# Kernel tuning notes

Measured on AMD Instinct MI355X. Metric: run time of the kernel, lower is better.

Reference implementation:

```python
import jax, jax.numpy as jnp
import numpy as np

B = 256          # graphs per batch
NN = 400         # ROI nodes per graph (N*(N-1)/2 = 79800 = input_dim)
HID = [32, 64, 128]
KS = [200, 100, 50]   # nodes kept after each TopKPooling (ratio 0.5 each)
EPS = 1e-5


def setup_inputs() -> dict:
    key = jax.random.key(0)
    ks = jax.random.split(key, 20)
    # flattened strict upper triangle of a nonnegative FC matrix per sample
    data = jax.random.uniform(ks[0], (B, NN * (NN - 1) // 2), dtype=jnp.float32)
    inp = {"data": data}
    dims = [1] + HID
    for l in range(3):
        fan_in = dims[l]
        inp[f"W{l+1}"] = jax.random.normal(ks[1 + 5 * l], (dims[l], dims[l + 1]), jnp.float32) / np.sqrt(fan_in)
        inp[f"b{l+1}"] = jnp.zeros((dims[l + 1],), jnp.float32)
        inp[f"g{l+1}"] = jnp.ones((dims[l + 1],), jnp.float32)      # BN gamma
        inp[f"be{l+1}"] = jnp.zeros((dims[l + 1],), jnp.float32)    # BN beta
        inp[f"p{l+1}"] = jax.random.normal(ks[4 + 5 * l], (dims[l + 1],), jnp.float32) * 0.1  # TopK score vector
    return inp


def _gcn_conv(A, X, W, b):
    # GCNConv with edge weights: add self loops (weight 1), symmetric D^-1/2 A D^-1/2
    n = A.shape[1]
    Al = A + jnp.eye(n, dtype=A.dtype)[None]          # (B, n, n)
    deg = Al.sum(axis=-1)                             # (B, n)
    dis = jnp.where(deg > 0, jax.lax.rsqrt(deg), 0.0)
    An = dis[:, :, None] * Al * dis[:, None, :]
    return jnp.einsum('bij,bjf->bif', An, X @ W) + b


def _block(A, X, W, b, g, be, p, k):
    # GCNConv -> ReLU -> BatchNorm(train stats) -> (dropout=identity) -> TopKPooling
    h = jax.nn.relu(_gcn_conv(A, X, W, b))
    mu = h.mean(axis=(0, 1))
    var = h.var(axis=(0, 1))
    h = (h - mu) * jax.lax.rsqrt(var + EPS) * g + be
    # TopKPooling: score = x . p / ||p||, keep top k per graph, gate by tanh(score)
    score = h @ p / jnp.linalg.norm(p)                # (B, n)
    vals, idx = jax.lax.top_k(score, k)               # (B, k)
    Xn = jnp.take_along_axis(h, idx[:, :, None], axis=1) * jnp.tanh(vals)[:, :, None]
    bi = jnp.arange(A.shape[0])[:, None, None]
    An = A[bi, idx[:, :, None], idx[:, None, :]]      # filter_adj: edges among kept nodes
    return An, Xn


def reference(data, W1, b1, g1, be1, p1, W2, b2, g2, be2, p2, W3, b3, g3, be3, p3):
    Bn = data.shape[0]
    iu0, iu1 = np.triu_indices(NN, 1)
    A = jnp.zeros((Bn, NN, NN), data.dtype).at[:, iu0, iu1].set(data)
    A = A + jnp.swapaxes(A, 1, 2)                     # symmetric FC adjacency, zero diag
    X = jnp.ones((Bn, NN, 1), data.dtype)             # initial node feature dim = 1
    A, X = _block(A, X, W1, b1, g1, be1, p1, KS[0])
    A, X = _block(A, X, W2, b2, g2, be2, p2, KS[1])
    A, X = _block(A, X, W3, b3, g3, be3, p3, KS[2])
    return X.max(axis=1)                              # global_max_pool -> (B, 128)
```

## Files before the change

### kernel.cpp

```cpp
#include <hip/hip_runtime.h>
#include <math.h>

#define BB   256
#define NN0  400
#define NE   79800
#define NTIL 28
#define EPSF 1e-5f

__device__ __forceinline__ int tri_e(int a, int c) {
  return a*(NN0-1) - ((a*(a-1))>>1) + (c - a - 1);
}

__device__ __forceinline__ size_t PRI(int b, int ti, int tj, int r) {
  return (((size_t)b*7 + ti)*7 + tj)*64 + r;
}

__device__ __forceinline__ float wave_sum(float v) {
  #pragma unroll
  for (int o = 32; o > 0; o >>= 1) v += __shfl_xor(v, o, 64);
  return v;
}

__device__ __forceinline__ void bitonic_desc(float* sc, int* si, int P) {
  const int tid = threadIdx.x;
  for (int k = 2; k <= P; k <<= 1) {
    for (int j = k >> 1; j > 0; j >>= 1) {
      __syncthreads();
      for (int i = tid; i < P; i += 256) {
        int ixj = i ^ j;
        if (ixj > i) {
          float a = sc[i], c = sc[ixj];
          int ai = si[i], ci = si[ixj];
          bool bef = (a > c) || (a == c && ai < ci);
          bool sw = ((i & k) == 0) ? !bef : bef;
          if (sw) { sc[i] = c; sc[ixj] = a; si[i] = ci; si[ixj] = ai; }
        }
      }
    }
  }
  __syncthreads();
}

__global__ __launch_bounds__(256) void k_tri_mv(
    const float* __restrict__ data, const float* __restrict__ disv,
    float* __restrict__ pr, float* __restrict__ pc) {
  __shared__ float tile[64][65];
  __shared__ float dI[64], dJ[64];
  const int q0 = blockIdx.x % 7, b = blockIdx.x / 7;
  const int tid = threadIdx.x;
  const int wave = tid >> 6, lane = tid & 63;
  const float* __restrict__ drow = data + (size_t)b*NE;
  int ti_a[4], tj_a[4];
  #pragma unroll
  for (int u = 0; u < 4; ++u) {
    int t = q0 + u*7;
    int ti = 0, rem = t;
    while (rem >= 7 - ti) { rem -= 7 - ti; ++ti; }
    ti_a[u] = ti; tj_a[u] = ti + rem;
  }
  float vreg[16];
  float rI = 0.f, rJ = 0.f;
  auto issue = [&](int u) {
    const int i0 = ti_a[u]*64, j0 = tj_a[u]*64;
    const int ni = min(64, NN0 - i0), nj = min(64, NN0 - j0);
    #pragma unroll
    for (int k = 0; k < 16; ++k) {
      const int rr = wave*16 + k;
      const int i = i0 + rr, j = j0 + lane;
      vreg[k] = 0.f;
      if (rr < ni && lane < nj && j > i) vreg[k] = drow[tri_e(i, j)];
    }
    if (disv) {
      if (tid < 64) rI = (tid < ni) ? disv[(size_t)b*NN0 + i0 + tid] : 0.f;
      else if (tid < 128) { const int c = tid-64; rJ = (c < nj) ? disv[(size_t)b*NN0 + j0 + c] : 0.f; }
    } else {
      if (tid < 64) rI = (tid < ni) ? 1.f : 0.f;
      else if (tid < 128) rJ = (tid-64 < nj) ? 1.f : 0.f;
    }
  };
  issue(0);
  #pragma unroll 1
  for (int u = 0; u < 4; ++u) {
    const int ti = ti_a[u], tj = tj_a[u];
    if (u) __syncthreads();
    #pragma unroll
    for (int k = 0; k < 16; ++k) tile[wave*16 + k][lane] = vreg[k];
    if (tid < 64) dI[tid] = rI;
    else if (tid < 128) dJ[tid-64] = rJ;
    __syncthreads();
    if (u + 1 < 4) issue(u + 1);
    {
      const int r = tid >> 2, q = tid & 3;
      float s = 0.f;
      #pragma unroll
      for (int c = 0; c < 16; ++c) s += tile[r][q*16 + c] * dJ[q*16 + c];
      s += __shfl_xor(s, 1, 64);
      s += __shfl_xor(s, 2, 64);
      if (q == 0) pr[PRI(b, ti, tj, r)] = s;
    }
    {
      const int c = tid >> 2, q = tid & 3;
      float s = 0.f;
      #pragma unroll
      for (int r = 0; r < 16; ++r) s += tile[q*16 + r][c] * dI[q*16 + r];
      s += __shfl_xor(s, 1, 64);
      s += __shfl_xor(s, 2, 64);
      if (q == 0) pc[PRI(b, ti, tj, c)] = s;
    }
  }
}

__global__ __launch_bounds__(256) void k_dis_red(
    const float* __restrict__ pr, const float* __restrict__ pc,
    float* __restrict__ dis1) {
  const int i = blockIdx.x*256 + threadIdx.x;
  const int b = i / NN0, n = i % NN0;
  const int t = n >> 6, r = n & 63;
  float acc = 1.f;
  for (int tj = t; tj < 7; ++tj) acc += pr[PRI(b, t, tj, r)];
  for (int ti = 0; ti <= t; ++ti) acc += pc[PRI(b, ti, t, r)];
  dis1[i] = rsqrtf(acc);
}

__global__ __launch_bounds__(256) void k_sfin_stats_red(
    const float* __restrict__ dis1,
    const float* __restrict__ pr, const float* __restrict__ pc,
    const float* __restrict__ W1, const float* __restrict__ b1,
    float* __restrict__ s1, float* __restrict__ part1) {
  __shared__ float sl[256];
  __shared__ float st[64];
  __shared__ float w1s[32], b1s[32];
  const int tid = threadIdx.x;
  const int i = blockIdx.x*256 + tid;
  if (tid < 32) { w1s[tid] = W1[tid]; b1s[tid] = b1[tid]; }
  if (tid < 64) st[tid] = 0.f;
  const int b = i / NN0, n = i % NN0;
  const int t = n >> 6, r = n & 63;
  float sacc = 0.f;
  for (int tj = t; tj < 7; ++tj) sacc += pr[PRI(b, t, tj, r)];
  for (int ti = 0; ti <= t; ++ti) sacc += pc[PRI(b, ti, t, r)];
  const float d = dis1[i];
  const float s = d * (d + sacc);
  s1[i] = s;
  sl[tid] = s;
  __syncthreads();
  const int f = tid & 31, sub = tid >> 5;
  const float w = w1s[f], bb = b1s[f];
  float S = 0.f, Q = 0.f;
  #pragma unroll
  for (int k = 0; k < 32; ++k) {
    const float ss = sl[sub*32 + k];
    const float h = fmaxf(ss*w + bb, 0.f);
    S += h; Q += h*h;
  }
  atomicAdd(&st[f], S);
  atomicAdd(&st[32+f], Q);
  __syncthreads();
  if (tid < 64) part1[(size_t)blockIdx.x*64 + tid] = st[tid];
}

__global__ void k_fin1(const float* __restrict__ part1, const float* __restrict__ g1,
                       const float* __restrict__ be1, const float* __restrict__ p1,
                       float* __restrict__ bn1) {
  const int tid = threadIdx.x;
  float scale = 0.f, shift = 0.f, pv = 0.f;
  if (tid < 32) {
    float S = 0.f, Q = 0.f;
    for (int blk = 0; blk < 400; ++blk) { S += part1[(size_t)blk*64 + tid]; Q += part1[(size_t)blk*64 + 32 + tid]; }
    const float N = 102400.f;
    const float mu = S / N;
    const float var = Q / N - mu*mu;
    const float inv = rsqrtf(var + EPSF);
    scale = inv * g1[tid];
    shift = be1[tid] - mu * scale;
    pv = p1[tid];
  }
  const float pn = sqrtf(wave_sum(pv*pv));
  if (tid < 32) { bn1[tid] = scale; bn1[32+tid] = shift; bn1[64+tid] = scale*pv/pn; }
  float u = (tid < 32) ? shift*pv/pn : 0.f;
  u = wave_sum(u);
  if (tid == 0) bn1[96] = u;
}

__global__ __launch_bounds__(256) void k_top1(
    const float* __restrict__ s1, const float* __restrict__ bn1,
    const float* __restrict__ W1, const float* __restrict__ b1,
    int* __restrict__ nodes2, int* __restrict__ sperm2, float* __restrict__ X2) {
  __shared__ float sc[512]; __shared__ int si[512];
  __shared__ float sS[NN0];
  __shared__ float tvs[200];
  __shared__ int nds_l[200];
  __shared__ float w1s[32], b1s[32], cfs[32], scs[32], shs[32];
  const int tid = threadIdx.x, b = blockIdx.x;
  if (tid < 32) {
    scs[tid] = bn1[tid]; shs[tid] = bn1[32+tid]; cfs[tid] = bn1[64+tid];
    w1s[tid] = W1[tid]; b1s[tid] = b1[tid];
  }
  __syncthreads();
  const float c0 = bn1[96];
  for (int i = tid; i < 512; i += 256) {
    if (i < NN0) {
      const float s = s1[(size_t)b*NN0 + i];
      sS[i] = s;
      float sco = c0;
      #pragma unroll
      for (int f = 0; f < 32; ++f) sco += fmaxf(s*w1s[f] + b1s[f], 0.f) * cfs[f];
      sc[i] = sco; si[i] = i;
    } else { sc[i] = -INFINITY; si[i] = 0x7fffffff; }
  }
  bitonic_desc(sc, si, 512);
  for (int k = tid; k < 200; k += 256) {
    tvs[k] = tanhf(sc[k]);
    nds_l[k] = si[k];
    nodes2[b*200 + k] = si[k];
  }
  __syncthreads();
  for (int o = tid; o < 6400; o += 256) {
    const int k = o >> 5, f = o & 31;
    const float s = sS[nds_l[k]];
    const float h = fmaxf(s*w1s[f] + b1s[f], 0.f);
    X2[(size_t)b*6400 + o] = (h*scs[f] + shs[f]) * tvs[k];
  }
  __syncthreads();
  if (tid < 256) {
    sc[tid] = (tid < 200) ? -(float)nds_l[tid] : -INFINITY;
    si[tid] = (tid < 200) ? tid : 0x7fffffff;
  }
  bitonic_desc(sc, si, 256);
  if (tid < 200) sperm2[b*200 + tid] = si[tid];
}

__global__ __launch_bounds__(256) void k_gatherA2(
    const float* __restrict__ data, const int* __restrict__ nodes2,
    const int* __restrict__ sperm2, float* __restrict__ A2, float* __restrict__ dis2) {
  __shared__ int nds[200], sp[200], sn[200];
  __shared__ float rowbuf[4][200];
  const int idx = blockIdx.x;
  const int r9 = idx >> 3;
  const int b = (idx & 7)*32 + r9/50;
  const int rg = r9 % 50;
  const int tid = threadIdx.x;
  if (tid < 200) { nds[tid] = nodes2[b*200 + tid]; sp[tid] = sperm2[b*200 + tid]; }
  __syncthreads();
  if (tid < 200) sn[tid] = nds[sp[tid]];
  __syncthreads();
  const int wave = tid >> 6, lane = tid & 63;
  const int i = rg*4 + wave;
  const int ni = nds[i];
  const float* __restrict__ drow = data + (size_t)b*NE;
  float accd = 0.f;
  for (int jj = lane; jj < 200; jj += 64) {
    const int sj = sn[jj];
    float v = 0.f;
    if (sj != ni) {
      const int a = min(ni, sj), c = max(ni, sj);
      v = drow[tri_e(a, c)];
    }
    rowbuf[wave][sp[jj]] = v;
    accd += v;
  }
  __syncthreads();
  for (int j = lane; j < 200; j += 64)
    A2[((size_t)b*200 + i)*200 + j] = rowbuf[wave][j];
  accd = wave_sum(accd);
  if (lane == 0) dis2[b*200 + i] = rsqrtf(1.f + accd);
}

__global__ __launch_bounds__(256) void k_Z2(
    const float* __restrict__ X2, const float* __restrict__ W2,
    const float* __restrict__ dis2, float* __restrict__ Z2) {
  __shared__ __align__(16) float xs[200*32];
  const int tid = threadIdx.x, b = blockIdx.x;
  const int f = tid & 63;
  float wr[32];
  #pragma unroll
  for (int c = 0; c < 32; ++c) wr[c] = W2[c*64 + f];
  for (int t = tid; t < 6400; t += 256) xs[t] = X2[(size_t)b*6400 + t];
  __syncthreads();
  for (int o = tid; o < 12800; o += 256) {
    const int j = o >> 6;
    float acc = 0.f;
    #pragma unroll
    for (int c4 = 0; c4 < 8; ++c4) {
      const float4 x4 = *(const float4*)&xs[(j<<5) + (c4<<2)];
      acc += x4.x*wr[c4*4] + x4.y*wr[c4*4+1] + x4.z*wr[c4*4+2] + x4.w*wr[c4*4+3];
    }
    Z2[(size_t)b*12800 + o] = dis2[b*200 + j] * acc;
  }
}

__global__ __launch_bounds__(256) void k_conv2(
    const float* __restrict__ A2, const float* __restrict__ Z2,
    const float* __restrict__ dis2, const float* __restrict__ b2,
    float* __restrict__ h2g, float* __restrict__ part2) {
  __shared__ __align__(16) float ab[40*64];
  __shared__ __align__(16) float zb[40*64];
  __shared__ float st[128];
  const int tid = threadIdx.x;
  const int b = blockIdx.x >> 2, p = blockIdx.x & 3;
  const int tx = tid & 15, ty = tid >> 4;
  if (tid < 128) st[tid] = 0.f;
  const float4 bv = *(const float4*)&b2[tx<<2];
  float acc[4][4] = {};
  #pragma unroll 1
  for (int j0 = 0; j0 < 200; j0 += 40) {
    __syncthreads();
    for (int t = tid; t < 640; t += 256) {
      const int js = t >> 4, f4 = t & 15;
      *(float4*)&zb[(js << 6) + (f4 << 2)] =
        *(const float4*)&Z2[((size_t)b*200 + (j0 + js))*64 + (f4 << 2)];
    }
    for (int t = tid; t < 640; t += 256) {
      const int js = t >> 4, c4l = t & 15;
      const int cg = (p << 6) + (c4l << 2);
      float4 v = make_float4(0.f, 0.f, 0.f, 0.f);
      if (cg < 200)
        v = *(const float4*)&A2[((size_t)b*200 + (j0 + js))*200 + cg];
      *(float4*)&ab[(js << 6) + (c4l << 2)] = v;
    }
    __syncthreads();
    #pragma unroll 2
    for (int js = 0; js < 40; ++js) {
      const float4 a4 = *(const float4*)&ab[(js << 6) + (ty << 2)];
      const float4 z4 = *(const float4*)&zb[(js << 6) + (tx << 2)];
      acc[0][0] += a4.x*z4.x; acc[0][1] += a4.x*z4.y; acc[0][2] += a4.x*z4.z; acc[0][3] += a4.x*z4.w;
      acc[1][0] += a4.y*z4.x; acc[1][1] += a4.y*z4.y; acc[1][2] += a4.y*z4.z; acc[1][3] += a4.y*z4.w;
      acc[2][0] += a4.z*z4.x; acc[2][1] += a4.z*z4.y; acc[2][2] += a4.z*z4.z; acc[2][3] += a4.z*z4.w;
      acc[3][0] += a4.w*z4.x; acc[3][1] += a4.w*z4.y; acc[3][2] += a4.w*z4.z; acc[3][3] += a4.w*z4.w;
    }
  }
  float ss[4] = {0,0,0,0}, qq[4] = {0,0,0,0};
  #pragma unroll
  for (int qr = 0; qr < 4; ++qr) {
    const int r = (p << 6) + (ty << 2) + qr;
    if (r < 200) {
      const float d = dis2[b*200 + r];
      const float4 zi = *(const float4*)&Z2[((size_t)b*200 + r)*64 + (tx << 2)];
      const float h0 = fmaxf(d*(acc[qr][0] + zi.x) + bv.x, 0.f);
      const float h1 = fmaxf(d*(acc[qr][1] + zi.y) + bv.y, 0.f);
      const float h2v = fmaxf(d*(acc[qr][2] + zi.z) + bv.z, 0.f);
      const float h3v = fmaxf(d*(acc[qr][3] + zi.w) + bv.w, 0.f);
      *(float4*)&h2g[((size_t)b*200 + r)*64 + (tx<<2)] = make_float4(h0,h1,h2v,h3v);
      ss[0]+=h0; ss[1]+=h1; ss[2]+=h2v; ss[3]+=h3v;
      qq[0]+=h0*h0; qq[1]+=h1*h1; qq[2]+=h2v*h2v; qq[3]+=h3v*h3v;
    }
  }
  #pragma unroll
  for (int qf = 0; qf < 4; ++qf) {
    atomicAdd(&st[(tx<<2)+qf], ss[qf]);
    atomicAdd(&st[64+(tx<<2)+qf], qq[qf]);
  }
  __syncthreads();
  if (tid < 128) part2[(size_t)blockIdx.x*128 + tid] = st[tid];
}

__global__ void k_fin2(const float* __restrict__ part2, const float* __restrict__ g2,
                       const float* __restrict__ be2, const float* __restrict__ p2,
                       float* __restrict__ bn2) {
  const int f = threadIdx.x;
  float S = 0.f, Q = 0.f;
  for (int blk = 0; blk < BB*4; ++blk) { S += part2[(size_t)blk*128 + f]; Q += part2[(size_t)blk*128 + 64 + f]; }
  const float N = 51200.f;
  const float mu = S/N, var = Q/N - mu*mu, inv = rsqrtf(var + EPSF);
  const float scale = inv*g2[f], shift = be2[f] - mu*scale;
  const float pv = p2[f];
  const float pn = sqrtf(wave_sum(pv*pv));
  bn2[f] = scale; bn2[64+f] = shift; bn2[128+f] = scale*pv/pn;
  const float u = wave_sum(shift*pv/pn);
  if (f == 0) bn2[192] = u;
}

__global__ __launch_bounds__(256) void k_top2(
    const float* __restrict__ h2g, const float* __restrict__ bn2,
    const int* __restrict__ nodes2, int* __restrict__ nodes3, float* __restrict__ X3) {
  __shared__ float sc[256]; __shared__ int si[256];
  const int tid = threadIdx.x, b = blockIdx.x;
  const int wave = tid >> 6, lane = tid & 63;
  const float cf = bn2[128 + lane];
  const float c20 = bn2[192];
  for (int i = wave; i < 200; i += 4) {
    float v = h2g[((size_t)b*200 + i)*64 + lane] * cf;
    v = wave_sum(v);
    if (lane == 0) { sc[i] = v + c20; si[i] = i; }
  }
  if (tid >= 200) { sc[tid] = -INFINITY; si[tid] = 0x7fffffff; }
  bitonic_desc(sc, si, 256);
  const float scale = bn2[lane], shift = bn2[64 + lane];
  for (int o = tid; o < 6400; o += 256) {
    const int k = o >> 6;
    const int idx = si[k];
    const float tv = tanhf(sc[k]);
    X3[(size_t)b*6400 + o] = (h2g[((size_t)b*200 + idx)*64 + lane] * scale + shift) * tv;
  }
  for (int k = tid; k < 100; k += 256) nodes3[b*100 + k] = nodes2[b*200 + si[k]];
}

__global__ __launch_bounds__(256) void k_gatherA3(
    const float* __restrict__ data, const int* __restrict__ nodes3,
    float* __restrict__ A3, float* __restrict__ dis3) {
  __shared__ int nds[100];
  const int b = blockIdx.x / 25, rg = blockIdx.x % 25;
  const int tid = threadIdx.x;
  if (tid < 100) nds[tid] = nodes3[b*100 + tid];
  __syncthreads();
  const int wave = tid >> 6, lane = tid & 63;
  const int i = rg*4 + wave;
  const int ni = nds[i];
  const float* __restrict__ drow = data + (size_t)b*NE;
  float accd = 0.f;
  for (int j = lane; j < 100; j += 64) {
    float v = 0.f;
    if (j != i) {
      const int nj = nds[j];
      const int a = min(ni, nj), c = max(ni, nj);
      v = drow[tri_e(a, c)];
    }
    A3[((size_t)b*100 + i)*100 + j] = v;
    accd += v;
  }
  accd = wave_sum(accd);
  if (lane == 0) dis3[b*100 + i] = rsqrtf(1.f + accd);
}

__global__ __launch_bounds__(256) void k_Z3(
    const float* __restrict__ X3, const float* __restrict__ W3,
    const float* __restrict__ dis3, float* __restrict__ Z3) {
  __shared__ __align__(16) float xs[100*64];
  const int tid = threadIdx.x, b = blockIdx.x;
  const int f = tid & 127;
  float wr[64];
  #pragma unroll
  for (int c = 0; c < 64; ++c) wr[c] = W3[c*128 + f];
  for (int t = tid; t < 6400; t += 256) xs[t] = X3[(size_t)b*6400 + t];
  __syncthreads();
  for (int o = tid; o < 12800; o += 256) {
    const int j = o >> 7;
    float acc = 0.f;
    #pragma unroll
    for (int c4 = 0; c4 < 16; ++c4) {
      const float4 x4 = *(const float4*)&xs[(j<<6) + (c4<<2)];
      acc += x4.x*wr[c4*4] + x4.y*wr[c4*4+1] + x4.z*wr[c4*4+2] + x4.w*wr[c4*4+3];
    }
    Z3[(size_t)b*12800 + o] = dis3[b*100 + j] * acc;
  }
}

__global__ __launch_bounds__(256) void k_conv3(
    const float* __restrict__ A3, const float* __restrict__ Z3,
    const float* __restrict__ dis3, const float* __restrict__ b3,
    float* __restrict__ h3g, float* __restrict__ part3) {
  __shared__ __align__(16) float z[100*128];
  __shared__ __align__(16) float ab[32*32];
  __shared__ float st[256];
  const int tid = threadIdx.x;
  const int b = blockIdx.x >> 2, p = blockIdx.x & 3;
  const int tx = tid & 31, ty = tid >> 5;
  for (int t = tid; t < 12800; t += 256) z[t] = Z3[(size_t)b*12800 + t];
  st[tid] = 0.f;
  const float4 bv = *(const float4*)&b3[tx<<2];
  float acc[4][4] = {};
  #pragma unroll 1
  for (int j0 = 0; j0 < 100; j0 += 32) {
    const int nj = (j0 + 32 <= 100) ? 32 : (100 - j0);
    __syncthreads();
    for (int t = tid; t < nj*32; t += 256) {
      const int js = t >> 5, lr = t & 31;
      const int c = (p << 5) + lr;
      ab[t] = (c < 100) ? A3[((size_t)b*100 + (j0 + js))*100 + c] : 0.f;
    }
    __syncthreads();
    for (int js = 0; js < nj; ++js) {
      const float4 a4 = *(const float4*)&ab[(js<<5) + (ty<<2)];
      const float4 z4 = *(const float4*)&z[((j0+js)<<7) + (tx<<2)];
      acc[0][0] += a4.x*z4.x; acc[0][1] += a4.x*z4.y; acc[0][2] += a4.x*z4.z; acc[0][3] += a4.x*z4.w;
      acc[1][0] += a4.y*z4.x; acc[1][1] += a4.y*z4.y; acc[1][2] += a4.y*z4.z; acc[1][3] += a4.y*z4.w;
      acc[2][0] += a4.z*z4.x; acc[2][1] += a4.z*z4.y; acc[2][2] += a4.z*z4.z; acc[2][3] += a4.z*z4.w;
      acc[3][0] += a4.w*z4.x; acc[3][1] += a4.w*z4.y; acc[3][2] += a4.w*z4.z; acc[3][3] += a4.w*z4.w;
    }
  }
  float ss[4] = {0,0,0,0}, qq[4] = {0,0,0,0};
  #pragma unroll
  for (int qr = 0; qr < 4; ++qr) {
    const int r = (p << 5) + (ty << 2) + qr;
    if (r < 100) {
      const float d = dis3[b*100 + r];
      const float4 zi = *(const float4*)&z[(r << 7) + (tx << 2)];
      const float h0 = fmaxf(d*(acc[qr][0] + zi.x) + bv.x, 0.f);
      const float h1 = fmaxf(d*(acc[qr][1] + zi.y) + bv.y, 0.f);
      const float h2v = fmaxf(d*(acc[qr][2] + zi.z) + bv.z, 0.f);
      const float h3v = fmaxf(d*(acc[qr][3] + zi.w) + bv.w, 0.f);
      *(float4*)&h3g[((size_t)b*100 + r)*128 + (tx<<2)] = make_float4(h0,h1,h2v,h3v);
      ss[0]+=h0; ss[1]+=h1; ss[2]+=h2v; ss[3]+=h3v;
      qq[0]+=h0*h0; qq[1]+=h1*h1; qq[2]+=h2v*h2v; qq[3]+=h3v*h3v;
    }
  }
  #pragma unroll
  for (int qf = 0; qf < 4; ++qf) {
    atomicAdd(&st[(tx<<2)+qf], ss[qf]);
    atomicAdd(&st[128+(tx<<2)+qf], qq[qf]);
  }
  __syncthreads();
  part3[(size_t)blockIdx.x*256 + tid] = st[tid];
}

__global__ void k_fin3(const float* __restrict__ part3, const float* __restrict__ g3,
                       const float* __restrict__ be3, const float* __restrict__ p3,
                       float* __restrict__ bn3) {
  __shared__ float red[2];
  const int f = threadIdx.x;
  const int wv = f >> 6, lane = f & 63;
  float S = 0.f, Q = 0.f;
  for (int blk = 0; blk < BB*4; ++blk) { S += part3[(size_t)blk*256 + f]; Q += part3[(size_t)blk*256 + 128 + f]; }
  const float N = 25600.f;
  const float mu = S/N, var = Q/N - mu*mu, inv = rsqrtf(var + EPSF);
  const float scale = inv*g3[f], shift = be3[f] - mu*scale;
  const float pv = p3[f];
  float t = wave_sum(pv*pv);
  if (lane == 0) red[wv] = t;
  __syncthreads();
  const float pn = sqrtf(red[0] + red[1]);
  bn3[f] = scale; bn3[128+f] = shift; bn3[256+f] = scale*pv/pn;
  float u = wave_sum(shift*pv/pn);
  __syncthreads();
  if (lane == 0) red[wv] = u;
  __syncthreads();
  if (f == 0) bn3[384] = red[0] + red[1];
}

__global__ __launch_bounds__(256) void k_top3(
    const float* __restrict__ h3g, const float* __restrict__ bn3, float* __restrict__ out) {
  __shared__ float sc[128]; __shared__ int si[128]; __shared__ float tv[64];
  const int tid = threadIdx.x, b = blockIdx.x;
  const int wave = tid >> 6, lane = tid & 63;
  const float clo = bn3[256 + lane], chi = bn3[320 + lane];
  const float c30 = bn3[384];
  for (int i = wave; i < 100; i += 4) {
    const float* hr = h3g + ((size_t)b*100 + i)*128;
    float v = hr[lane]*clo + hr[64 + lane]*chi;
    v = wave_sum(v);
    if (lane == 0) { sc[i] = v + c30; si[i] = i; }
  }
  if (tid >= 100 && tid < 128) { sc[tid] = -INFINITY; si[tid] = 0x7fffffff; }
  bitonic_desc(sc, si, 128);
  if (tid < 50) tv[tid] = tanhf(sc[tid]);
  __syncthreads();
  if (tid < 128) {
    const float scale = bn3[tid], shift = bn3[128 + tid];
    float m = -INFINITY;
    for (int k = 0; k < 50; ++k) {
      const float h = h3g[((size_t)b*100 + si[k])*128 + tid];
      m = fmaxf(m, (h*scale + shift)*tv[k]);
    }
    out[(size_t)b*128 + tid] = m;
  }
}

extern "C" void kernel_launch(void* const* d_in, const int* in_sizes, int n_in,
                              void* d_out, int out_size, void* d_ws, size_t ws_size,
                              hipStream_t stream) {
  (void)in_sizes; (void)n_in; (void)out_size; (void)ws_size;
  const float* data = (const float*)d_in[0];
  const float* W1 = (const float*)d_in[1];
  const float* b1 = (const float*)d_in[2];
  const float* g1 = (const float*)d_in[3];
  const float* be1 = (const float*)d_in[4];
  const float* p1 = (const float*)d_in[5];
  const float* W2 = (const float*)d_in[6];
  const float* b2 = (const float*)d_in[7];
  const float* g2 = (const float*)d_in[8];
  const float* be2 = (const float*)d_in[9];
  const float* p2 = (const float*)d_in[10];
  const float* W3 = (const float*)d_in[11];
  const float* b3 = (const float*)d_in[12];
  const float* g3 = (const float*)d_in[13];
  const float* be3 = (const float*)d_in[14];
  const float* p3 = (const float*)d_in[15];
  float* out = (float*)d_out;

  char* ws = (char*)d_ws;
  size_t off = 0;
  auto alloc = [&](size_t n) { size_t o = off; off += (n + 255) & ~(size_t)255; return o; };
  float* pr     = (float*)(ws + alloc((size_t)BB*49*64*4));
  float* pc     = (float*)(ws + alloc((size_t)BB*49*64*4));
  float* dis1   = (float*)(ws + alloc((size_t)BB*NN0*4));
  float* s1     = (float*)(ws + alloc((size_t)BB*NN0*4));
  float* part1  = (float*)(ws + alloc((size_t)400*64*4));
  float* bn1    = (float*)(ws + alloc(128*4));
  int*   nodes2 = (int*)  (ws + alloc((size_t)BB*200*4));
  int*   sperm2 = (int*)  (ws + alloc((size_t)BB*200*4));
  float* X2     = (float*)(ws + alloc((size_t)BB*6400*4));
  char*  big    =          ws + alloc((size_t)BB*40000*4);
  float* A2     = (float*)big;
  float* X3     = (float*)big;
  float* A3     = (float*)(big + (size_t)BB*6400*4);
  float* Z3     = (float*)(big + (size_t)BB*6400*4 + (size_t)BB*10000*4);
  float* dis2   = (float*)(ws + alloc((size_t)BB*200*4));
  float* Z2     = (float*)(ws + alloc((size_t)BB*12800*4));
  float* h2     = (float*)(ws + alloc((size_t)BB*12800*4));
  float* part2  = (float*)(ws + alloc((size_t)BB*4*128*4));
  float* bn2    = (float*)(ws + alloc(256*4));
  int*   nodes3 = (int*)  (ws + alloc((size_t)BB*100*4));
  float* dis3   = (float*)(ws + alloc((size_t)BB*100*4));
  float* h3     = (float*)(ws + alloc((size_t)BB*12800*4));
  float* part3  = (float*)(ws + alloc((size_t)BB*4*256*4));
  float* bn3    = (float*)(ws + alloc(512*4));

  k_tri_mv<<<dim3(BB*7), dim3(256), 0, stream>>>(data, nullptr, pr, pc);
  k_dis_red<<<dim3(400), dim3(256), 0, stream>>>(pr, pc, dis1);
  k_tri_mv<<<dim3(BB*7), dim3(256), 0, stream>>>(data, dis1, pr, pc);
  k_sfin_stats_red<<<dim3(400), dim3(256), 0, stream>>>(dis1, pr, pc, W1, b1, s1, part1);
  k_fin1<<<dim3(1), dim3(64), 0, stream>>>(part1, g1, be1, p1, bn1);
  k_top1<<<dim3(BB), dim3(256), 0, stream>>>(s1, bn1, W1, b1, nodes2, sperm2, X2);
  k_gatherA2<<<dim3(BB*50), dim3(256), 0, stream>>>(data, nodes2, sperm2, A2, dis2);
  k_Z2<<<dim3(BB), dim3(256), 0, stream>>>(X2, W2, dis2, Z2);
  k_conv2<<<dim3(BB*4), dim3(256), 0, stream>>>(A2, Z2, dis2, b2, h2, part2);
  k_fin2<<<dim3(1), dim3(64), 0, stream>>>(part2, g2, be2, p2, bn2);
  k_top2<<<dim3(BB), dim3(256), 0, stream>>>(h2, bn2, nodes2, nodes3, X3);
  k_gatherA3<<<dim3(BB*25), dim3(256), 0, stream>>>(data, nodes3, A3, dis3);
  k_Z3<<<dim3(BB), dim3(256), 0, stream>>>(X3, W3, dis3, Z3);
  k_conv3<<<dim3(BB*4), dim3(256), 0, stream>>>(A3, Z3, dis3, b3, h3, part3);
  k_fin3<<<dim3(1), dim3(128), 0, stream>>>(part3, g3, be3, p3, bn3);
  k_top3<<<dim3(BB), dim3(256), 0, stream>>>(h3, bn3, out);
}
```

Before: 505.8 us.

## Fuse BN finalize, degree reduction and feature transforms into neighbouring kernels

Removes the k_dis_red, k_fin1/2/3 and k_Z2/Z3 launches. Degree normalisation is recomputed inside the second tri_mv pass and in the stats kernel. BN statistics are accumulated with global atomics into a memset buffer and finalized at the start of each top-k kernel. The XW matmuls move into the top-k kernels, with the dis scaling applied later in the conv kernels. This cuts launch overhead, the single-block serial reductions and intermediate round trips, at the cost of redundant per-block work, nondeterministic atomic ordering, and one extra pr/pc buffer pair.

```diff
diff --git a/kernel.cpp b/kernel.cpp
--- a/kernel.cpp
+++ b/kernel.cpp
@@ -4,7 +4,6 @@
 #define BB   256
 #define NN0  400
 #define NE   79800
-#define NTIL 28
 #define EPSF 1e-5f
 
 __device__ __forceinline__ int tri_e(int a, int c) {
@@ -42,7 +41,8 @@
 }
 
 __global__ __launch_bounds__(256) void k_tri_mv(
-    const float* __restrict__ data, const float* __restrict__ disv,
+    const float* __restrict__ data,
+    const float* __restrict__ pr_in, const float* __restrict__ pc_in,
     float* __restrict__ pr, float* __restrict__ pc) {
   __shared__ float tile[64][65];
   __shared__ float dI[64], dJ[64];
@@ -70,12 +70,32 @@
       vreg[k] = 0.f;
       if (rr < ni && lane < nj && j > i) vreg[k] = drow[tri_e(i, j)];
     }
-    if (disv) {
-      if (tid < 64) rI = (tid < ni) ? disv[(size_t)b*NN0 + i0 + tid] : 0.f;
-      else if (tid < 128) { const int c = tid-64; rJ = (c < nj) ? disv[(size_t)b*NN0 + j0 + c] : 0.f; }
+    if (pr_in) {
+      if (tid < 64) {
+        float a = 0.f;
+        if (tid < ni) {
+          const int tt = ti_a[u], r = tid;
+          float acc = 1.f;
+          for (int tj = tt; tj < 7; ++tj) acc += pr_in[PRI(b, tt, tj, r)];
+          for (int ts = 0; ts <= tt; ++ts) acc += pc_in[PRI(b, ts, tt, r)];
+          a = rsqrtf(acc);
+        }
+        rI = a;
+      } else if (tid < 128) {
+        const int c = tid - 64;
+        float a = 0.f;
+        if (c < nj) {
+          const int tt = tj_a[u], r = c;
+          float acc = 1.f;
+          for (int tj = tt; tj < 7; ++tj) acc += pr_in[PRI(b, tt, tj, r)];
+          for (int ts = 0; ts <= tt; ++ts) acc += pc_in[PRI(b, ts, tt, r)];
+          a = rsqrtf(acc);
+        }
+        rJ = a;
+      }
     } else {
       if (tid < 64) rI = (tid < ni) ? 1.f : 0.f;
-      else if (tid < 128) rJ = (tid-64 < nj) ? 1.f : 0.f;
+      else if (tid < 128) rJ = (tid - 64 < nj) ? 1.f : 0.f;
     }
   };
   issue(0);
@@ -110,23 +130,11 @@
   }
 }
 
-__global__ __launch_bounds__(256) void k_dis_red(
+__global__ __launch_bounds__(256) void k_sfin_stats_red(
     const float* __restrict__ pr, const float* __restrict__ pc,
-    float* __restrict__ dis1) {
-  const int i = blockIdx.x*256 + threadIdx.x;
-  const int b = i / NN0, n = i % NN0;
-  const int t = n >> 6, r = n & 63;
-  float acc = 1.f;
-  for (int tj = t; tj < 7; ++tj) acc += pr[PRI(b, t, tj, r)];
-  for (int ti = 0; ti <= t; ++ti) acc += pc[PRI(b, ti, t, r)];
-  dis1[i] = rsqrtf(acc);
-}
-
-__global__ __launch_bounds__(256) void k_sfin_stats_red(
-    const float* __restrict__ dis1,
-    const float* __restrict__ pr, const float* __restrict__ pc,
+    const float* __restrict__ pr2, const float* __restrict__ pc2,
     const float* __restrict__ W1, const float* __restrict__ b1,
-    float* __restrict__ s1, float* __restrict__ part1) {
+    float* __restrict__ s1, float* __restrict__ acc1) {
   __shared__ float sl[256];
   __shared__ float st[64];
   __shared__ float w1s[32], b1s[32];
@@ -136,10 +144,10 @@
   if (tid < 64) st[tid] = 0.f;
   const int b = i / NN0, n = i % NN0;
   const int t = n >> 6, r = n & 63;
-  float sacc = 0.f;
-  for (int tj = t; tj < 7; ++tj) sacc += pr[PRI(b, t, tj, r)];
-  for (int ti = 0; ti <= t; ++ti) sacc += pc[PRI(b, ti, t, r)];
-  const float d = dis1[i];
+  float dacc = 1.f, sacc = 0.f;
+  for (int tj = t; tj < 7; ++tj) { dacc += pr[PRI(b, t, tj, r)]; sacc += pr2[PRI(b, t, tj, r)]; }
+  for (int ti = 0; ti <= t; ++ti) { dacc += pc[PRI(b, ti, t, r)]; sacc += pc2[PRI(b, ti, t, r)]; }
+  const float d = rsqrtf(dacc);
   const float s = d * (d + sacc);
   s1[i] = s;
   sl[tid] = s;
@@ -156,48 +164,44 @@
   atomicAdd(&st[f], S);
   atomicAdd(&st[32+f], Q);
   __syncthreads();
-  if (tid < 64) part1[(size_t)blockIdx.x*64 + tid] = st[tid];
-}
-
-__global__ void k_fin1(const float* __restrict__ part1, const float* __restrict__ g1,
-                       const float* __restrict__ be1, const float* __restrict__ p1,
-                       float* __restrict__ bn1) {
-  const int tid = threadIdx.x;
-  float scale = 0.f, shift = 0.f, pv = 0.f;
-  if (tid < 32) {
-    float S = 0.f, Q = 0.f;
-    for (int blk = 0; blk < 400; ++blk) { S += part1[(size_t)blk*64 + tid]; Q += part1[(size_t)blk*64 + 32 + tid]; }
-    const float N = 102400.f;
-    const float mu = S / N;
-    const float var = Q / N - mu*mu;
-    const float inv = rsqrtf(var + EPSF);
-    scale = inv * g1[tid];
-    shift = be1[tid] - mu * scale;
-    pv = p1[tid];
-  }
-  const float pn = sqrtf(wave_sum(pv*pv));
-  if (tid < 32) { bn1[tid] = scale; bn1[32+tid] = shift; bn1[64+tid] = scale*pv/pn; }
-  float u = (tid < 32) ? shift*pv/pn : 0.f;
-  u = wave_sum(u);
-  if (tid == 0) bn1[96] = u;
+  if (tid < 64) atomicAdd(&acc1[tid], st[tid]);
 }
 
 __global__ __launch_bounds__(256) void k_top1(
-    const float* __restrict__ s1, const float* __restrict__ bn1,
+    const float* __restrict__ s1, const float* __restrict__ acc1,
     const float* __restrict__ W1, const float* __restrict__ b1,
-    int* __restrict__ nodes2, int* __restrict__ sperm2, float* __restrict__ X2) {
+    const float* __restrict__ g1, const float* __restrict__ be1,
+    const float* __restrict__ p1, const float* __restrict__ W2,
+    int* __restrict__ nodes2, int* __restrict__ sperm2, float* __restrict__ Y2) {
   __shared__ float sc[512]; __shared__ int si[512];
   __shared__ float sS[NN0];
   __shared__ float tvs[200];
   __shared__ int nds_l[200];
   __shared__ float w1s[32], b1s[32], cfs[32], scs[32], shs[32];
+  __shared__ __align__(16) float hp[6400];
+  __shared__ float c0s;
   const int tid = threadIdx.x, b = blockIdx.x;
-  if (tid < 32) {
-    scs[tid] = bn1[tid]; shs[tid] = bn1[32+tid]; cfs[tid] = bn1[64+tid];
-    w1s[tid] = W1[tid]; b1s[tid] = b1[tid];
-  }
-  __syncthreads();
-  const float c0 = bn1[96];
+  if (tid < 32) { w1s[tid] = W1[tid]; b1s[tid] = b1[tid]; }
+  if (tid < 64) {
+    float scale = 0.f, shift = 0.f, pv = 0.f;
+    if (tid < 32) {
+      const float S = acc1[tid], Q = acc1[32 + tid];
+      const float N = 102400.f;
+      const float mu = S / N;
+      const float var = Q / N - mu*mu;
+      const float inv = rsqrtf(var + EPSF);
+      scale = inv * g1[tid];
+      shift = be1[tid] - mu * scale;
+      pv = p1[tid];
+    }
+    const float pn = sqrtf(wave_sum(pv*pv));
+    if (tid < 32) { scs[tid] = scale; shs[tid] = shift; cfs[tid] = scale*pv/pn; }
+    float u = (tid < 32) ? shift*pv/pn : 0.f;
+    u = wave_sum(u);
+    if (tid == 0) c0s = u;
+  }
+  __syncthreads();
+  const float c0 = c0s;
   for (int i = tid; i < 512; i += 256) {
     if (i < NN0) {
       const float s = s1[(size_t)b*NN0 + i];
@@ -219,7 +223,24 @@
     const int k = o >> 5, f = o & 31;
     const float s = sS[nds_l[k]];
     const float h = fmaxf(s*w1s[f] + b1s[f], 0.f);
-    X2[(size_t)b*6400 + o] = (h*scs[f] + shs[f]) * tvs[k];
+    hp[o] = (h*scs[f] + shs[f]) * tvs[k];
+  }
+  __syncthreads();
+  {
+    const int g = tid & 63;
+    float wr[32];
+    #pragma unroll
+    for (int f = 0; f < 32; ++f) wr[f] = W2[f*64 + g];
+    for (int o = tid; o < 12800; o += 256) {
+      const int k = o >> 6;
+      float acc = 0.f;
+      #pragma unroll
+      for (int c4 = 0; c4 < 8; ++c4) {
+        const float4 x4 = *(const float4*)&hp[(k<<5) + (c4<<2)];
+        acc += x4.x*wr[c4*4] + x4.y*wr[c4*4+1] + x4.z*wr[c4*4+2] + x4.w*wr[c4*4+3];
+      }
+      Y2[(size_t)b*12800 + o] = acc;
+    }
   }
   __syncthreads();
   if (tid < 256) {
@@ -266,33 +287,10 @@
   if (lane == 0) dis2[b*200 + i] = rsqrtf(1.f + accd);
 }
 
-__global__ __launch_bounds__(256) void k_Z2(
-    const float* __restrict__ X2, const float* __restrict__ W2,
-    const float* __restrict__ dis2, float* __restrict__ Z2) {
-  __shared__ __align__(16) float xs[200*32];
-  const int tid = threadIdx.x, b = blockIdx.x;
-  const int f = tid & 63;
-  float wr[32];
-  #pragma unroll
-  for (int c = 0; c < 32; ++c) wr[c] = W2[c*64 + f];
-  for (int t = tid; t < 6400; t += 256) xs[t] = X2[(size_t)b*6400 + t];
-  __syncthreads();
-  for (int o = tid; o < 12800; o += 256) {
-    const int j = o >> 6;
-    float acc = 0.f;
-    #pragma unroll
-    for (int c4 = 0; c4 < 8; ++c4) {
-      const float4 x4 = *(const float4*)&xs[(j<<5) + (c4<<2)];
-      acc += x4.x*wr[c4*4] + x4.y*wr[c4*4+1] + x4.z*wr[c4*4+2] + x4.w*wr[c4*4+3];
-    }
-    Z2[(size_t)b*12800 + o] = dis2[b*200 + j] * acc;
-  }
-}
-
 __global__ __launch_bounds__(256) void k_conv2(
-    const float* __restrict__ A2, const float* __restrict__ Z2,
+    const float* __restrict__ A2, const float* __restrict__ Y2,
     const float* __restrict__ dis2, const float* __restrict__ b2,
-    float* __restrict__ h2g, float* __restrict__ part2) {
+    float* __restrict__ h2g, float* __restrict__ acc2g) {
   __shared__ __align__(16) float ab[40*64];
   __shared__ __align__(16) float zb[40*64];
   __shared__ float st[128];
@@ -307,8 +305,10 @@
     __syncthreads();
     for (int t = tid; t < 640; t += 256) {
       const int js = t >> 4, f4 = t & 15;
-      *(float4*)&zb[(js << 6) + (f4 << 2)] =
-        *(const float4*)&Z2[((size_t)b*200 + (j0 + js))*64 + (f4 << 2)];
+      const float dz = dis2[b*200 + j0 + js];
+      float4 v = *(const float4*)&Y2[((size_t)b*200 + (j0 + js))*64 + (f4 << 2)];
+      v.x *= dz; v.y *= dz; v.z *= dz; v.w *= dz;
+      *(float4*)&zb[(js << 6) + (f4 << 2)] = v;
     }
     for (int t = tid; t < 640; t += 256) {
       const int js = t >> 4, c4l = t & 15;
@@ -335,11 +335,12 @@
     const int r = (p << 6) + (ty << 2) + qr;
     if (r < 200) {
       const float d = dis2[b*200 + r];
-      const float4 zi = *(const float4*)&Z2[((size_t)b*200 + r)*64 + (tx << 2)];
-      const float h0 = fmaxf(d*(acc[qr][0] + zi.x) + bv.x, 0.f);
-      const float h1 = fmaxf(d*(acc[qr][1] + zi.y) + bv.y, 0.f);
-      const float h2v = fmaxf(d*(acc[qr][2] + zi.z) + bv.z, 0.f);
-      const float h3v = fmaxf(d*(acc[qr][3] + zi.w) + bv.w, 0.f);
+      const float dd = d*d;
+      const float4 zi = *(const float4*)&Y2[((size_t)b*200 + r)*64 + (tx << 2)];
+      const float h0 = fmaxf(d*acc[qr][0] + dd*zi.x + bv.x, 0.f);
+      const float h1 = fmaxf(d*acc[qr][1] + dd*zi.y + bv.y, 0.f);
+      const float h2v = fmaxf(d*acc[qr][2] + dd*zi.z + bv.z, 0.f);
+      const float h3v = fmaxf(d*acc[qr][3] + dd*zi.w + bv.w, 0.f);
       *(float4*)&h2g[((size_t)b*200 + r)*64 + (tx<<2)] = make_float4(h0,h1,h2v,h3v);
       ss[0]+=h0; ss[1]+=h1; ss[2]+=h2v; ss[3]+=h3v;
       qq[0]+=h0*h0; qq[1]+=h1*h1; qq[2]+=h2v*h2v; qq[3]+=h3v*h3v;
@@ -351,33 +352,35 @@
     atomicAdd(&st[64+(tx<<2)+qf], qq[qf]);
   }
   __syncthreads();
-  if (tid < 128) part2[(size_t)blockIdx.x*128 + tid] = st[tid];
-}
-
-__global__ void k_fin2(const float* __restrict__ part2, const float* __restrict__ g2,
-                       const float* __restrict__ be2, const float* __restrict__ p2,
-                       float* __restrict__ bn2) {
-  const int f = threadIdx.x;
-  float S = 0.f, Q = 0.f;
-  for (int blk = 0; blk < BB*4; ++blk) { S += part2[(size_t)blk*128 + f]; Q += part2[(size_t)blk*128 + 64 + f]; }
-  const float N = 51200.f;
-  const float mu = S/N, var = Q/N - mu*mu, inv = rsqrtf(var + EPSF);
-  const float scale = inv*g2[f], shift = be2[f] - mu*scale;
-  const float pv = p2[f];
-  const float pn = sqrtf(wave_sum(pv*pv));
-  bn2[f] = scale; bn2[64+f] = shift; bn2[128+f] = scale*pv/pn;
-  const float u = wave_sum(shift*pv/pn);
-  if (f == 0) bn2[192] = u;
+  if (tid < 128) atomicAdd(&acc2g[tid], st[tid]);
 }
 
 __global__ __launch_bounds__(256) void k_top2(
-    const float* __restrict__ h2g, const float* __restrict__ bn2,
-    const int* __restrict__ nodes2, int* __restrict__ nodes3, float* __restrict__ X3) {
+    const float* __restrict__ h2g, const float* __restrict__ acc2,
+    const float* __restrict__ g2, const float* __restrict__ be2,
+    const float* __restrict__ p2, const float* __restrict__ W3,
+    const int* __restrict__ nodes2, int* __restrict__ nodes3,
+    float* __restrict__ Y3) {
   __shared__ float sc[256]; __shared__ int si[256];
+  __shared__ __align__(16) float xs[6400];
+  __shared__ float sc2[64], sh2[64], cf2[64];
+  __shared__ float c20s;
   const int tid = threadIdx.x, b = blockIdx.x;
+  if (tid < 64) {
+    const float S = acc2[tid], Q = acc2[64 + tid];
+    const float N = 51200.f;
+    const float mu = S/N, var = Q/N - mu*mu, inv = rsqrtf(var + EPSF);
+    const float scale = inv*g2[tid], shift = be2[tid] - mu*scale;
+    const float pv = p2[tid];
+    const float pn = sqrtf(wave_sum(pv*pv));
+    sc2[tid] = scale; sh2[tid] = shift; cf2[tid] = scale*pv/pn;
+    const float u = wave_sum(shift*pv/pn);
+    if (tid == 0) c20s = u;
+  }
+  __syncthreads();
   const int wave = tid >> 6, lane = tid & 63;
-  const float cf = bn2[128 + lane];
-  const float c20 = bn2[192];
+  const float cf = cf2[lane];
+  const float c20 = c20s;
   for (int i = wave; i < 200; i += 4) {
     float v = h2g[((size_t)b*200 + i)*64 + lane] * cf;
     v = wave_sum(v);
@@ -385,14 +388,31 @@
   }
   if (tid >= 200) { sc[tid] = -INFINITY; si[tid] = 0x7fffffff; }
   bitonic_desc(sc, si, 256);
-  const float scale = bn2[lane], shift = bn2[64 + lane];
+  const float scale = sc2[lane], shift = sh2[lane];
   for (int o = tid; o < 6400; o += 256) {
     const int k = o >> 6;
     const int idx = si[k];
     const float tv = tanhf(sc[k]);
-    X3[(size_t)b*6400 + o] = (h2g[((size_t)b*200 + idx)*64 + lane] * scale + shift) * tv;
+    xs[o] = (h2g[((size_t)b*200 + idx)*64 + lane] * scale + shift) * tv;
   }
   for (int k = tid; k < 100; k += 256) nodes3[b*100 + k] = nodes2[b*200 + si[k]];
+  __syncthreads();
+  {
+    const int g = tid & 127;
+    float wr[64];
+    #pragma unroll
+    for (int f = 0; f < 64; ++f) wr[f] = W3[f*128 + g];
+    for (int o = tid; o < 12800; o += 256) {
+      const int k = o >> 7;
+      float acc = 0.f;
+      #pragma unroll
+      for (int c4 = 0; c4 < 16; ++c4) {
+        const float4 x4 = *(const float4*)&xs[(k<<6) + (c4<<2)];
+        acc += x4.x*wr[c4*4] + x4.y*wr[c4*4+1] + x4.z*wr[c4*4+2] + x4.w*wr[c4*4+3];
+      }
+      Y3[(size_t)b*12800 + o] = acc;
+    }
+  }
 }
 
 __global__ __launch_bounds__(256) void k_gatherA3(
@@ -422,40 +442,18 @@
   if (lane == 0) dis3[b*100 + i] = rsqrtf(1.f + accd);
 }
 
-__global__ __launch_bounds__(256) void k_Z3(
-    const float* __restrict__ X3, const float* __restrict__ W3,
-    const float* __restrict__ dis3, float* __restrict__ Z3) {
-  __shared__ __align__(16) float xs[100*64];
-  const int tid = threadIdx.x, b = blockIdx.x;
-  const int f = tid & 127;
-  float wr[64];
-  #pragma unroll
-  for (int c = 0; c < 64; ++c) wr[c] = W3[c*128 + f];
-  for (int t = tid; t < 6400; t += 256) xs[t] = X3[(size_t)b*6400 + t];
-  __syncthreads();
-  for (int o = tid; o < 12800; o += 256) {
-    const int j = o >> 7;
-    float acc = 0.f;
-    #pragma unroll
-    for (int c4 = 0; c4 < 16; ++c4) {
-      const float4 x4 = *(const float4*)&xs[(j<<6) + (c4<<2)];
-      acc += x4.x*wr[c4*4] + x4.y*wr[c4*4+1] + x4.z*wr[c4*4+2] + x4.w*wr[c4*4+3];
-    }
-    Z3[(size_t)b*12800 + o] = dis3[b*100 + j] * acc;
-  }
-}
-
 __global__ __launch_bounds__(256) void k_conv3(
-    const float* __restrict__ A3, const float* __restrict__ Z3,
+    const float* __restrict__ A3, const float* __restrict__ Y3,
     const float* __restrict__ dis3, const float* __restrict__ b3,
-    float* __restrict__ h3g, float* __restrict__ part3) {
+    float* __restrict__ h3g, float* __restrict__ acc3g) {
   __shared__ __align__(16) float z[100*128];
   __shared__ __align__(16) float ab[32*32];
   __shared__ float st[256];
   const int tid = threadIdx.x;
   const int b = blockIdx.x >> 2, p = blockIdx.x & 3;
   const int tx = tid & 31, ty = tid >> 5;
-  for (int t = tid; t < 12800; t += 256) z[t] = Z3[(size_t)b*12800 + t];
+  for (int t = tid; t < 12800; t += 256)
+    z[t] = Y3[(size_t)b*12800 + t] * dis3[b*100 + (t >> 7)];
   st[tid] = 0.f;
   const float4 bv = *(const float4*)&b3[tx<<2];
   float acc[4][4] = {};
@@ -500,40 +498,37 @@
     atomicAdd(&st[128+(tx<<2)+qf], qq[qf]);
   }
   __syncthreads();
-  part3[(size_t)blockIdx.x*256 + tid] = st[tid];
-}
-
-__global__ void k_fin3(const float* __restrict__ part3, const float* __restrict__ g3,
-                       const float* __restrict__ be3, const float* __restrict__ p3,
-                       float* __restrict__ bn3) {
-  __shared__ float red[2];
-  const int f = threadIdx.x;
-  const int wv = f >> 6, lane = f & 63;
-  float S = 0.f, Q = 0.f;
-  for (int blk = 0; blk < BB*4; ++blk) { S += part3[(size_t)blk*256 + f]; Q += part3[(size_t)blk*256 + 128 + f]; }
-  const float N = 25600.f;
-  const float mu = S/N, var = Q/N - mu*mu, inv = rsqrtf(var + EPSF);
-  const float scale = inv*g3[f], shift = be3[f] - mu*scale;
-  const float pv = p3[f];
-  float t = wave_sum(pv*pv);
-  if (lane == 0) red[wv] = t;
-  __syncthreads();
-  const float pn = sqrtf(red[0] + red[1]);
-  bn3[f] = scale; bn3[128+f] = shift; bn3[256+f] = scale*pv/pn;
-  float u = wave_sum(shift*pv/pn);
-  __syncthreads();
-  if (lane == 0) red[wv] = u;
-  __syncthreads();
-  if (f == 0) bn3[384] = red[0] + red[1];
+  atomicAdd(&acc3g[tid], st[tid]);
 }
 
 __global__ __launch_bounds__(256) void k_top3(
-    const float* __restrict__ h3g, const float* __restrict__ bn3, float* __restrict__ out) {
+    const float* __restrict__ h3g, const float* __restrict__ acc3,
+    const float* __restrict__ g3, const float* __restrict__ be3,
+    const float* __restrict__ p3, float* __restrict__ out) {
   __shared__ float sc[128]; __shared__ int si[128]; __shared__ float tv[64];
+  __shared__ float scl[128], shl[128], cfl[128];
+  __shared__ float red2[4];
   const int tid = threadIdx.x, b = blockIdx.x;
   const int wave = tid >> 6, lane = tid & 63;
-  const float clo = bn3[256 + lane], chi = bn3[320 + lane];
-  const float c30 = bn3[384];
+  float scale = 0.f, shift = 0.f, pv = 0.f;
+  if (tid < 128) {
+    const float S = acc3[tid], Q = acc3[128 + tid];
+    const float N = 25600.f;
+    const float mu = S/N, var = Q/N - mu*mu, inv = rsqrtf(var + EPSF);
+    scale = inv*g3[tid]; shift = be3[tid] - mu*scale; pv = p3[tid];
+    const float t2 = wave_sum(pv*pv);
+    if (lane == 0) red2[wave] = t2;
+  }
+  __syncthreads();
+  const float pn = sqrtf(red2[0] + red2[1]);
+  if (tid < 128) {
+    scl[tid] = scale; shl[tid] = shift; cfl[tid] = scale*pv/pn;
+    const float u = wave_sum(shift*pv/pn);
+    if (lane == 0) red2[2 + wave] = u;
+  }
+  __syncthreads();
+  const float c30 = red2[2] + red2[3];
+  const float clo = cfl[lane], chi = cfl[64 + lane];
   for (int i = wave; i < 100; i += 4) {
     const float* hr = h3g + ((size_t)b*100 + i)*128;
     float v = hr[lane]*clo + hr[64 + lane]*chi;
@@ -545,11 +540,11 @@
   if (tid < 50) tv[tid] = tanhf(sc[tid]);
   __syncthreads();
   if (tid < 128) {
-    const float scale = bn3[tid], shift = bn3[128 + tid];
+    const float scalev = scl[tid], shiftv = shl[tid];
     float m = -INFINITY;
     for (int k = 0; k < 50; ++k) {
       const float h = h3g[((size_t)b*100 + si[k])*128 + tid];
-      m = fmaxf(m, (h*scale + shift)*tv[k]);
+      m = fmaxf(m, (h*scalev + shiftv)*tv[k]);
     }
     out[(size_t)b*128 + tid] = m;
   }
@@ -582,43 +577,34 @@
   auto alloc = [&](size_t n) { size_t o = off; off += (n + 255) & ~(size_t)255; return o; };
   float* pr     = (float*)(ws + alloc((size_t)BB*49*64*4));
   float* pc     = (float*)(ws + alloc((size_t)BB*49*64*4));
-  float* dis1   = (float*)(ws + alloc((size_t)BB*NN0*4));
+  float* pr2    = (float*)(ws + alloc((size_t)BB*49*64*4));
+  float* pc2    = (float*)(ws + alloc((size_t)BB*49*64*4));
   float* s1     = (float*)(ws + alloc((size_t)BB*NN0*4));
-  float* part1  = (float*)(ws + alloc((size_t)400*64*4));
-  float* bn1    = (float*)(ws + alloc(128*4));
+  float* accz   = (float*)(ws + alloc(448*4));
   int*   nodes2 = (int*)  (ws + alloc((size_t)BB*200*4));
   int*   sperm2 = (int*)  (ws + alloc((size_t)BB*200*4));
-  float* X2     = (float*)(ws + alloc((size_t)BB*6400*4));
-  char*  big    =          ws + alloc((size_t)BB*40000*4);
-  float* A2     = (float*)big;
-  float* X3     = (float*)big;
-  float* A3     = (float*)(big + (size_t)BB*6400*4);
-  float* Z3     = (float*)(big + (size_t)BB*6400*4 + (size_t)BB*10000*4);
+  float* Y2     = (float*)(ws + alloc((size_t)BB*12800*4));
+  float* A2     = (float*)(ws + alloc((size_t)BB*40000*4));
   float* dis2   = (float*)(ws + alloc((size_t)BB*200*4));
-  float* Z2     = (float*)(ws + alloc((size_t)BB*12800*4));
   float* h2     = (float*)(ws + alloc((size_t)BB*12800*4));
-  float* part2  = (float*)(ws + alloc((size_t)BB*4*128*4));
-  float* bn2    = (float*)(ws + alloc(256*4));
   int*   nodes3 = (int*)  (ws + alloc((size_t)BB*100*4));
+  float* Y3     = (float*)(ws + alloc((size_t)BB*12800*4));
+  float* A3     = (float*)(ws + alloc((size_t)BB*10000*4));
   float* dis3   = (float*)(ws + alloc((size_t)BB*100*4));
   float* h3     = (float*)(ws + alloc((size_t)BB*12800*4));
-  float* part3  = (float*)(ws + alloc((size_t)BB*4*256*4));
-  float* bn3    = (float*)(ws + alloc(512*4));
-
-  k_tri_mv<<<dim3(BB*7), dim3(256), 0, stream>>>(data, nullptr, pr, pc);
-  k_dis_red<<<dim3(400), dim3(256), 0, stream>>>(pr, pc, dis1);
-  k_tri_mv<<<dim3(BB*7), dim3(256), 0, stream>>>(data, dis1, pr, pc);
-  k_sfin_stats_red<<<dim3(400), dim3(256), 0, stream>>>(dis1, pr, pc, W1, b1, s1, part1);
-  k_fin1<<<dim3(1), dim3(64), 0, stream>>>(part1, g1, be1, p1, bn1);
-  k_top1<<<dim3(BB), dim3(256), 0, stream>>>(s1, bn1, W1, b1, nodes2, sperm2, X2);
+  float* acc1 = accz;
+  float* acc2 = accz + 64;
+  float* acc3 = accz + 192;
+
+  hipMemsetAsync(accz, 0, 448*4, stream);
+  k_tri_mv<<<dim3(BB*7), dim3(256), 0, stream>>>(data, nullptr, nullptr, pr, pc);
+  k_tri_mv<<<dim3(BB*7), dim3(256), 0, stream>>>(data, pr, pc, pr2, pc2);
+  k_sfin_stats_red<<<dim3(400), dim3(256), 0, stream>>>(pr, pc, pr2, pc2, W1, b1, s1, acc1);
+  k_top1<<<dim3(BB), dim3(256), 0, stream>>>(s1, acc1, W1, b1, g1, be1, p1, W2, nodes2, sperm2, Y2);
   k_gatherA2<<<dim3(BB*50), dim3(256), 0, stream>>>(data, nodes2, sperm2, A2, dis2);
-  k_Z2<<<dim3(BB), dim3(256), 0, stream>>>(X2, W2, dis2, Z2);
-  k_conv2<<<dim3(BB*4), dim3(256), 0, stream>>>(A2, Z2, dis2, b2, h2, part2);
-  k_fin2<<<dim3(1), dim3(64), 0, stream>>>(part2, g2, be2, p2, bn2);
-  k_top2<<<dim3(BB), dim3(256), 0, stream>>>(h2, bn2, nodes2, nodes3, X3);
+  k_conv2<<<dim3(BB*4), dim3(256), 0, stream>>>(A2, Y2, dis2, b2, h2, acc2);
+  k_top2<<<dim3(BB), dim3(256), 0, stream>>>(h2, acc2, g2, be2, p2, W3, nodes2, nodes3, Y3);
   k_gatherA3<<<dim3(BB*25), dim3(256), 0, stream>>>(data, nodes3, A3, dis3);
-  k_Z3<<<dim3(BB), dim3(256), 0, stream>>>(X3, W3, dis3, Z3);
-  k_conv3<<<dim3(BB*4), dim3(256), 0, stream>>>(A3, Z3, dis3, b3, h3, part3);
-  k_fin3<<<dim3(1), dim3(128), 0, stream>>>(part3, g3, be3, p3, bn3);
-  k_top3<<<dim3(BB), dim3(256), 0, stream>>>(h3, bn3, out);
-}
+  k_conv3<<<dim3(BB*4), dim3(256), 0, stream>>>(A3, Y3, dis3, b3, h3, acc3);
+  k_top3<<<dim3(BB), dim3(256), 0, stream>>>(h3, acc3, g3, be3, p3, out);
+}
```

New measurement: 466.1 us. -7.8%, faster.
